# Kernel optimization log

Measured on AMD Instinct MI355X. Metric: run time of the kernel, lower is better.

Reference implementation:

```python
import jax, jax.numpy as jnp
import numpy as np

HID = 32      # STGAT hidden_dim
HEADS = 8
NHID = HID // HEADS  # per-head hidden = 4
NEG_SLOPE = 0.2


def lstm_layer(x, Wih, Whh, bih, bhh):
    # x: (BN, T, H_in); torch gate order i, f, g, o
    BN = x.shape[0]
    H = Whh.shape[1]
    b = bih + bhh

    def step(carry, xt):
        h, c = carry
        z = xt @ Wih.T + h @ Whh.T + b
        i, f, g, o = jnp.split(z, 4, axis=-1)
        c = jax.nn.sigmoid(f) * c + jax.nn.sigmoid(i) * jnp.tanh(g)
        h = jax.nn.sigmoid(o) * jnp.tanh(c)
        return (h, c), h

    h0 = jnp.zeros((BN, H), x.dtype)
    _, ys = jax.lax.scan(step, (h0, h0), jnp.swapaxes(x, 0, 1))
    return jnp.swapaxes(ys, 0, 1)  # (BN, T, H)


def setup_inputs():
    key = jax.random.key(0)
    ks = jax.random.split(key, 16)
    B, N, T_in, F_in = 8, 300, 12, 3
    T_out, F_out = 12, 3
    X = jax.random.normal(ks[0], (B, N, T_in, F_in), jnp.float32)
    adj = (jax.random.uniform(ks[1], (N, N)) < 0.05).astype(jnp.float32)
    A_hat = jnp.maximum(adj, jnp.eye(N, dtype=jnp.float32))  # self-loops

    def init(k, shape, fan):
        return jax.random.normal(k, shape, jnp.float32) / np.float32(np.sqrt(fan))

    W_gat = init(ks[2], (HID, F_in), F_in)          # linear (no bias)
    a_attn = init(ks[3], (2 * NHID,), 2 * NHID)     # attn (no bias), flattened (1, 2*nhid)
    W_ih0 = init(ks[4], (4 * HID, HID), HID)
    W_hh0 = init(ks[5], (4 * HID, HID), HID)
    b_ih0 = init(ks[6], (4 * HID,), HID)
    b_hh0 = init(ks[7], (4 * HID,), HID)
    W_ih1 = init(ks[8], (4 * HID, HID), HID)
    W_hh1 = init(ks[9], (4 * HID, HID), HID)
    b_ih1 = init(ks[10], (4 * HID,), HID)
    b_hh1 = init(ks[11], (4 * HID,), HID)
    fc_W = init(ks[12], (F_out * T_out, HID), HID)
    fc_b = init(ks[13], (F_out * T_out,), HID)
    return {"A_hat": A_hat, "X": X, "W_gat": W_gat, "a_attn": a_attn,
            "W_ih0": W_ih0, "W_hh0": W_hh0, "b_ih0": b_ih0, "b_hh0": b_hh0,
            "W_ih1": W_ih1, "W_hh1": W_hh1, "b_ih1": b_ih1, "b_hh1": b_hh1,
            "fc_W": fc_W, "fc_b": fc_b}


def reference(A_hat, X, W_gat, a_attn, W_ih0, W_hh0, b_ih0, b_hh0,
              W_ih1, W_hh1, b_ih1, b_hh1, fc_W, fc_b):
    B, N, T, F = X.shape
    T_out = fc_W.shape[0] // F  # nums_feature_output == F here

    # --- GAT, vectorized over (batch, timestep) ---
    # g: (B, N, T, HEADS, NHID)
    g = (X @ W_gat.T).reshape(B, N, T, HEADS, NHID)
    a_l, a_r = a_attn[:NHID], a_attn[NHID:]
    # attn(g_concat) = a_l . g_i + a_r . g_j  (exact split of the concat+linear)
    gl = jnp.einsum('bithd,d->bith', g, a_l)
    gr = jnp.einsum('bjthd,d->bjth', g, a_r)
    e = jax.nn.leaky_relu(gl[:, :, None] + gr[:, None, :], NEG_SLOPE)  # (B,i,j,T,H)
    mask = (A_hat == 0)[None, :, :, None, None]
    e = jnp.where(mask, -jnp.inf, e)
    a = jax.nn.softmax(e, axis=2)  # softmax over j (dim=1 of the (i,j,h) tensor)
    h_gat = jnp.einsum('bijth,bjthd->bithd', a, g).reshape(B, N, T, HID)

    # --- 2-layer LSTM over time, per (b, n) sequence ---
    lstm_in = h_gat.reshape(B * N, T, HID)
    h1 = lstm_layer(lstm_in, W_ih0, W_hh0, b_ih0, b_hh0)
    h2 = lstm_layer(h1, W_ih1, W_hh1, b_ih1, b_hh1)
    h_last = h2[:, -1, :]  # (B*N, HID)

    out = h_last @ fc_W.T + fc_b
    return out.reshape(B, N, T_out, F)
```

## Files before the change

kernel.cpp:

```cpp
#include <hip/hip_runtime.h>

typedef __attribute__((ext_vector_type(8))) short s8v;
typedef __attribute__((ext_vector_type(4))) float f4v;

__device__ __forceinline__ float sgm(float x) { return 1.f / (1.f + __expf(-x)); }
__device__ __forceinline__ float tanhq(float x) { return 2.f / (1.f + __expf(-2.f*x)) - 1.f; }
__device__ __forceinline__ void bsplit(float x, short& hi, short& lo) {
    unsigned u = __float_as_uint(x);
    unsigned hb = u & 0xffff0000u;
    hi = (short)(hb >> 16);
    float r = x - __uint_as_float(hb);
    lo = (short)(__float_as_uint(r) >> 16);
}
__device__ __forceinline__ float dppadd1(float x) {
    return x + __uint_as_float(__builtin_amdgcn_mov_dpp(__float_as_uint(x), 0xB1, 0xF, 0xF, true));
}
__device__ __forceinline__ float dppadd2(float x) {
    return x + __uint_as_float(__builtin_amdgcn_mov_dpp(__float_as_uint(x), 0x4E, 0xF, 0xF, true));
}

#define SQ 5

__device__ __forceinline__ void zA2(const short* vh, const short* vl,
    const s8v (&ah)[2][2], const s8v (&al)[2][2], const f4v (&bias)[2],
    int boff, int g, f4v& dA, f4v& dB)
{
    s8v bh0 = *(const s8v*)((const char*)vh + boff +      g*16);
    s8v bh1 = *(const s8v*)((const char*)vh + boff + 64 + g*16);
    s8v bl0 = *(const s8v*)((const char*)vl + boff +      g*16);
    s8v bl1 = *(const s8v*)((const char*)vl + boff + 64 + g*16);
    dA = bias[0];
    dA = __builtin_amdgcn_mfma_f32_16x16x32_bf16(ah[0][0], bh0, dA, 0, 0, 0);
    dA = __builtin_amdgcn_mfma_f32_16x16x32_bf16(ah[0][1], bh1, dA, 0, 0, 0);
    dA = __builtin_amdgcn_mfma_f32_16x16x32_bf16(al[0][0], bh0, dA, 0, 0, 0);
    dA = __builtin_amdgcn_mfma_f32_16x16x32_bf16(al[0][1], bh1, dA, 0, 0, 0);
    dA = __builtin_amdgcn_mfma_f32_16x16x32_bf16(ah[0][0], bl0, dA, 0, 0, 0);
    dA = __builtin_amdgcn_mfma_f32_16x16x32_bf16(ah[0][1], bl1, dA, 0, 0, 0);
    dB = bias[1];
    dB = __builtin_amdgcn_mfma_f32_16x16x32_bf16(ah[1][0], bh0, dB, 0, 0, 0);
    dB = __builtin_amdgcn_mfma_f32_16x16x32_bf16(ah[1][1], bh1, dB, 0, 0, 0);
    dB = __builtin_amdgcn_mfma_f32_16x16x32_bf16(al[1][0], bh0, dB, 0, 0, 0);
    dB = __builtin_amdgcn_mfma_f32_16x16x32_bf16(al[1][1], bh1, dB, 0, 0, 0);
    dB = __builtin_amdgcn_mfma_f32_16x16x32_bf16(ah[1][0], bl0, dB, 0, 0, 0);
    dB = __builtin_amdgcn_mfma_f32_16x16x32_bf16(ah[1][1], bl1, dB, 0, 0, 0);
}

__global__ __launch_bounds__(512, 4) void k_stgat(
    const float* __restrict__ A,    const float* __restrict__ X,
    const float* __restrict__ Wg,   const float* __restrict__ aat,
    const float* __restrict__ Wih0, const float* __restrict__ Whh0,
    const float* __restrict__ bih0, const float* __restrict__ bhh0,
    const float* __restrict__ Wih1, const float* __restrict__ Whh1,
    const float* __restrict__ bih1, const float* __restrict__ bhh1,
    const float* __restrict__ fcW,  const float* __restrict__ fcb,
    float* __restrict__ out)
{
    __shared__ int   snbr[SQ][64];
    __shared__ int   scnt[SQ];
    __shared__ float shg[SQ*384];
    __shared__ __align__(16) char uarea[43200];

    const int tid  = threadIdx.x;
    const int w    = tid >> 6;
    const int l    = tid & 63;
    const int seq0 = blockIdx.x * SQ;
    const int b    = seq0 / 300, i0 = seq0 - b*300;

    float* Xs = (float*)uarea;

    {
        const float* Xg = X + (size_t)b * 10800;
        for (int x = tid; x < 10800; x += 512) Xs[x] = Xg[x];
    }
    if (w < SQ) {
        int i = i0 + w;
        int c = 0;
        for (int j0 = 0; j0 < 300; j0 += 64) {
            int j = j0 + l;
            bool p = (j < 300) && (A[i*300 + j] != 0.f);
            unsigned long long m = __ballot(p);
            if (p) {
                int pos = __popcll(m & ((1ull << l) - 1ull));
                if (c + pos < 64) snbr[w][c + pos] = j;
            }
            c += __popcll(m);
        }
        if (c > 64) c = 64;
        if (l == 0) scnt[w] = c;
    }
    __syncthreads();

    {
        const int hh = l >> 3, j8 = l & 7, dd = j8 & 3;
        float wal0=0.f, wal1=0.f, wal2=0.f, war0=0.f, war1=0.f, war2=0.f;
        #pragma unroll
        for (int d4 = 0; d4 < 4; d4++) {
            float av = aat[d4], bv = aat[4+d4];
            const float* wr = Wg + (hh*4+d4)*3;
            wal0 += wr[0]*av; wal1 += wr[1]*av; wal2 += wr[2]*av;
            war0 += wr[0]*bv; war1 += wr[1]*bv; war2 += wr[2]*bv;
        }
        const float* wp = Wg + (hh*4+dd)*3;
        float wp0 = wp[0], wp1 = wp[1], wp2 = wp[2];

        for (int u = 7 - w; u < SQ*12; u += 8) {
            int us = u / 12, t = u - us*12;
            int i = i0 + us;
            int c = scnt[us];

            const float* Xi = Xs + i*36 + t*3;
            float gl = Xi[0]*wal0 + Xi[1]*wal1 + Xi[2]*wal2;

            float s = 0.f, a0 = 0.f, a1 = 0.f, a2 = 0.f;
            for (int kk = j8; kk < c; kk += 8) {
                int j = snbr[us][kk];
                const float* Xj = Xs + j*36 + t*3;
                float y0 = Xj[0], y1 = Xj[1], y2 = Xj[2];
                float e = gl + y0*war0 + y1*war1 + y2*war2;
                e = e > 0.f ? e : 0.2f*e;
                float wt = __expf(e);
                s += wt; a0 += wt*y0; a1 += wt*y1; a2 += wt*y2;
            }
            s  = dppadd1(s);  a0 = dppadd1(a0); a1 = dppadd1(a1); a2 = dppadd1(a2);
            s  = dppadd2(s);  a0 = dppadd2(a0); a1 = dppadd2(a1); a2 = dppadd2(a2);
            s  += __shfl_xor(s, 4, 64);
            a0 += __shfl_xor(a0, 4, 64);
            a1 += __shfl_xor(a1, 4, 64);
            a2 += __shfl_xor(a2, 4, 64);
            if (j8 < 4)
                shg[us*384 + t*32 + hh*4 + dd] = (a0*wp0 + a1*wp1 + a2*wp2) / s;
        }
    }

    const int n16 = l & 15;
    const int g   = l >> 4;
    const int cA  = w*8 + g;
    const int cB  = w*8 + 4 + g;
    s8v a0h[2][2], a0l[2][2], a1h[2][2], a1l[2][2];
    f4v bias0[2], bias1[2];
    if (w < 4) {
        #pragma unroll
        for (int tau = 0; tau < 2; tau++) {
            const int arow = (n16 & 3)*32 + w*8 + tau*4 + (n16 >> 2);
            const float* s00 = Wih0 + arow*32 + g*8;
            const float* s01 = Whh0 + arow*32 + g*8;
            const float* s10 = Wih1 + arow*32 + g*8;
            const float* s11 = Whh1 + arow*32 + g*8;
            #pragma unroll
            for (int j = 0; j < 8; j++) {
                short hh2, ll2;
                bsplit(s00[j], hh2, ll2); a0h[tau][0][j]=hh2; a0l[tau][0][j]=ll2;
                bsplit(s01[j], hh2, ll2); a0h[tau][1][j]=hh2; a0l[tau][1][j]=ll2;
                bsplit(s10[j], hh2, ll2); a1h[tau][0][j]=hh2; a1l[tau][0][j]=ll2;
                bsplit(s11[j], hh2, ll2); a1h[tau][1][j]=hh2; a1l[tau][1][j]=ll2;
            }
            const int cell = w*8 + tau*4 + g;
            #pragma unroll
            for (int r = 0; r < 4; r++) {
                bias0[tau][r] = bih0[r*32+cell] + bhh0[r*32+cell];
                bias1[tau][r] = bih1[r*32+cell] + bhh1[r*32+cell];
            }
        }
    }
    __syncthreads();

    short* vh0 = (short*)uarea;
    short* vl0 = vh0 + 16*72;
    short* vh1 = vl0 + 16*72;
    short* vl1 = vh1 + 16*72;
    float* sh1f = (float*)(vl1 + 16*72);

    {
        unsigned* vz = (unsigned*)uarea;
        for (int x = tid; x < 2304; x += 512) vz[x] = 0;
    }
    __syncthreads();
    if (tid >= 256 && tid < 416) {
        int us = (tid - 256) >> 5, uc = tid & 31;
        short hh2, ll2; bsplit(shg[us*384 + uc], hh2, ll2);
        vh0[us*72 + uc] = hh2;  vl0[us*72 + uc] = ll2;
    }
    __syncthreads();

    const int boff = n16 * 144;
    float c0A = 0.f, c0B = 0.f, c1A = 0.f, c1B = 0.f;

    auto cellup = [&](f4v z, float& cs) -> float {
        cs = sgm(z[1])*cs + sgm(z[0])*tanhq(z[2]);
        return sgm(z[3])*tanhq(cs);
    };
    auto wr_h0 = [&](float hv, int c) {
        short hh2, ll2; bsplit(hv, hh2, ll2);
        vh0[n16*72 + 32 + c] = hh2;  vl0[n16*72 + 32 + c] = ll2;
        vh1[n16*72 + c]      = hh2;  vl1[n16*72 + c]      = ll2;
    };
    auto wr_h1 = [&](float hv, int c) {
        short hh2, ll2; bsplit(hv, hh2, ll2);
        vh1[n16*72 + 32 + c] = hh2;  vl1[n16*72 + 32 + c] = ll2;
    };

    {
        f4v zpA, zpB;
        if (w < 4) zA2(vh0, vl0, a0h, a0l, bias0, boff, g, zpA, zpB);
        __syncthreads();
        if (w < 4) {
            wr_h0(cellup(zpA, c0A), cA);
            wr_h0(cellup(zpB, c0B), cB);
        }
        if (tid >= 256 && tid < 416) {
            int us = (tid - 256) >> 5, uc = tid & 31;
            short hh2, ll2; bsplit(shg[us*384 + 32 + uc], hh2, ll2);
            vh0[us*72 + uc] = hh2;  vl0[us*72 + uc] = ll2;
        }
        __syncthreads();
    }

    for (int t = 0; t < 12; t++) {
        f4v z1A, z1B, z0A, z0B;
        if (w < 4) {
            zA2(vh1, vl1, a1h, a1l, bias1, boff, g, z1A, z1B);
            if (t < 11)
                zA2(vh0, vl0, a0h, a0l, bias0, boff, g, z0A, z0B);
        }
        __syncthreads();
        if (w < 4) {
            float h1a = cellup(z1A, c1A);
            float h1b = cellup(z1B, c1B);
            wr_h1(h1a, cA);  wr_h1(h1b, cB);
            if (t == 11) {
                if (n16 < SQ) { sh1f[n16*32 + cA] = h1a; sh1f[n16*32 + cB] = h1b; }
            } else {
                wr_h0(cellup(z0A, c0A), cA);
                wr_h0(cellup(z0B, c0B), cB);
            }
        }
        if (tid >= 256 && tid < 416 && t < 10) {
            int us = (tid - 256) >> 5, uc = tid & 31;
            short hh2, ll2; bsplit(shg[us*384 + (t+2)*32 + uc], hh2, ll2);
            vh0[us*72 + uc] = hh2;  vl0[us*72 + uc] = ll2;
        }
        __syncthreads();
    }

    if (tid < SQ*36) {
        int s = tid / 36, r = tid - s*36;
        float acc = fcb[r];
        #pragma unroll
        for (int c4 = 0; c4 < 8; c4++) {
            float4 uv = *(const float4*)&fcW[r*32 + 4*c4];
            acc += uv.x*sh1f[s*32+4*c4+0] + uv.y*sh1f[s*32+4*c4+1]
                 + uv.z*sh1f[s*32+4*c4+2] + uv.w*sh1f[s*32+4*c4+3];
        }
        out[(seq0 + s)*36 + r] = acc;
    }
}

extern "C" void kernel_launch(void* const* d_in, const int* in_sizes, int n_in,
                              void* d_out, int out_size, void* d_ws, size_t ws_size,
                              hipStream_t stream)
{
    const float* A    = (const float*)d_in[0];
    const float* X    = (const float*)d_in[1];
    const float* Wg   = (const float*)d_in[2];
    const float* aat  = (const float*)d_in[3];
    const float* Wih0 = (const float*)d_in[4];
    const float* Whh0 = (const float*)d_in[5];
    const float* bih0 = (const float*)d_in[6];
    const float* bhh0 = (const float*)d_in[7];
    const float* Wih1 = (const float*)d_in[8];
    const float* Whh1 = (const float*)d_in[9];
    const float* bih1 = (const float*)d_in[10];
    const float* bhh1 = (const float*)d_in[11];
    const float* fcW  = (const float*)d_in[12];
    const float* fcb  = (const float*)d_in[13];
    float* out = (float*)d_out;

    k_stgat<<<480, 512, 0, stream>>>(A, X, Wg, aat,
                                     Wih0, Whh0, bih0, bhh0,
                                     Wih1, Whh1, bih1, bhh1,
                                     fcW, fcb, out);
}
```

Measured before the change: 36.82 us.

## Split LSTM layers across warp groups with double-buffered hidden-state staging

Instead of waves 0-3 computing both LSTM layers while waves 4-7 sit idle, waves 0-3 now run layer 0 and waves 4-7 run layer 1 concurrently, each holding only one layer's split-bf16 weights. The hidden-state LDS buffers are double-buffered by parity, so each wavefront step needs one barrier instead of two. This should halve the per-step MFMA and cell-update work per wave and cut barriers. The cost is doubled LDS for the state buffers and more duplicate stores, since layer-0 output is written into both layers' buffers.

```diff
diff --git a/kernel.cpp b/kernel.cpp
--- a/kernel.cpp
+++ b/kernel.cpp
@@ -132,114 +132,114 @@
         }
     }
 
-    const int n16 = l & 15;
-    const int g   = l >> 4;
-    const int cA  = w*8 + g;
-    const int cB  = w*8 + 4 + g;
-    s8v a0h[2][2], a0l[2][2], a1h[2][2], a1l[2][2];
-    f4v bias0[2], bias1[2];
-    if (w < 4) {
+    const int n16   = l & 15;
+    const int g     = l >> 4;
+    const int wl    = w & 3;
+    const int layer = w >> 2;
+    const int cA    = wl*8 + g;
+    const int cB    = wl*8 + 4 + g;
+    s8v ah[2][2], al[2][2];
+    f4v bias[2];
+    {
+        const float* Wih = layer ? Wih1 : Wih0;
+        const float* Whh = layer ? Whh1 : Whh0;
+        const float* bi  = layer ? bih1 : bih0;
+        const float* bh  = layer ? bhh1 : bhh0;
         #pragma unroll
         for (int tau = 0; tau < 2; tau++) {
-            const int arow = (n16 & 3)*32 + w*8 + tau*4 + (n16 >> 2);
-            const float* s00 = Wih0 + arow*32 + g*8;
-            const float* s01 = Whh0 + arow*32 + g*8;
-            const float* s10 = Wih1 + arow*32 + g*8;
-            const float* s11 = Whh1 + arow*32 + g*8;
+            const int arow = (n16 & 3)*32 + wl*8 + tau*4 + (n16 >> 2);
+            const float* si = Wih + arow*32 + g*8;
+            const float* sh = Whh + arow*32 + g*8;
             #pragma unroll
             for (int j = 0; j < 8; j++) {
-                short hh2, ll2;
-                bsplit(s00[j], hh2, ll2); a0h[tau][0][j]=hh2; a0l[tau][0][j]=ll2;
-                bsplit(s01[j], hh2, ll2); a0h[tau][1][j]=hh2; a0l[tau][1][j]=ll2;
-                bsplit(s10[j], hh2, ll2); a1h[tau][0][j]=hh2; a1l[tau][0][j]=ll2;
-                bsplit(s11[j], hh2, ll2); a1h[tau][1][j]=hh2; a1l[tau][1][j]=ll2;
-            }
-            const int cell = w*8 + tau*4 + g;
+                short h2, l2;
+                bsplit(si[j], h2, l2); ah[tau][0][j]=h2; al[tau][0][j]=l2;
+                bsplit(sh[j], h2, l2); ah[tau][1][j]=h2; al[tau][1][j]=l2;
+            }
+            const int cell = wl*8 + tau*4 + g;
             #pragma unroll
-            for (int r = 0; r < 4; r++) {
-                bias0[tau][r] = bih0[r*32+cell] + bhh0[r*32+cell];
-                bias1[tau][r] = bih1[r*32+cell] + bhh1[r*32+cell];
-            }
-        }
-    }
-    __syncthreads();
-
-    short* vh0 = (short*)uarea;
-    short* vl0 = vh0 + 16*72;
-    short* vh1 = vl0 + 16*72;
-    short* vl1 = vh1 + 16*72;
-    float* sh1f = (float*)(vl1 + 16*72);
-
-    {
-        unsigned* vz = (unsigned*)uarea;
-        for (int x = tid; x < 2304; x += 512) vz[x] = 0;
-    }
-    __syncthreads();
-    if (tid >= 256 && tid < 416) {
-        int us = (tid - 256) >> 5, uc = tid & 31;
-        short hh2, ll2; bsplit(shg[us*384 + uc], hh2, ll2);
-        vh0[us*72 + uc] = hh2;  vl0[us*72 + uc] = ll2;
+            for (int r = 0; r < 4; r++)
+                bias[tau][r] = bi[r*32+cell] + bh[r*32+cell];
+        }
+    }
+    __syncthreads();
+
+    short* vb = (short*)uarea;
+    float* sh1f = (float*)(vb + 8*1152);
+    #define VOFF(buf, lay, hl) ((((buf)*2 + (lay))*2 + (hl))*1152)
+
+    { unsigned* vz = (unsigned*)uarea; for (int x = tid; x < 4608; x += 512) vz[x] = 0; }
+    __syncthreads();
+    if (tid < SQ*32) {
+        int us = tid >> 5, uc = tid & 31;
+        short h2, l2; bsplit(shg[us*384 + uc], h2, l2);
+        vb[VOFF(0,0,0) + us*72 + uc] = h2;  vb[VOFF(0,0,1) + us*72 + uc] = l2;
     }
     __syncthreads();
 
     const int boff = n16 * 144;
-    float c0A = 0.f, c0B = 0.f, c1A = 0.f, c1B = 0.f;
+    float csA = 0.f, csB = 0.f;
+    int cur = 0;
 
     auto cellup = [&](f4v z, float& cs) -> float {
         cs = sgm(z[1])*cs + sgm(z[0])*tanhq(z[2]);
         return sgm(z[3])*tanhq(cs);
     };
-    auto wr_h0 = [&](float hv, int c) {
-        short hh2, ll2; bsplit(hv, hh2, ll2);
-        vh0[n16*72 + 32 + c] = hh2;  vl0[n16*72 + 32 + c] = ll2;
-        vh1[n16*72 + c]      = hh2;  vl1[n16*72 + c]      = ll2;
-    };
-    auto wr_h1 = [&](float hv, int c) {
-        short hh2, ll2; bsplit(hv, hh2, ll2);
-        vh1[n16*72 + 32 + c] = hh2;  vl1[n16*72 + 32 + c] = ll2;
-    };
-
-    {
-        f4v zpA, zpB;
-        if (w < 4) zA2(vh0, vl0, a0h, a0l, bias0, boff, g, zpA, zpB);
+
+    {
+        if (layer == 0) {
+            f4v zAa, zBb;
+            zA2(vb + VOFF(0,0,0), vb + VOFF(0,0,1), ah, al, bias, boff, g, zAa, zBb);
+            float hA = cellup(zAa, csA);
+            float hB = cellup(zBb, csB);
+            short h2, l2;
+            bsplit(hA, h2, l2);
+            vb[VOFF(1,0,0) + n16*72 + 32 + cA] = h2;  vb[VOFF(1,0,1) + n16*72 + 32 + cA] = l2;
+            vb[VOFF(1,1,0) + n16*72 + cA]      = h2;  vb[VOFF(1,1,1) + n16*72 + cA]      = l2;
+            bsplit(hB, h2, l2);
+            vb[VOFF(1,0,0) + n16*72 + 32 + cB] = h2;  vb[VOFF(1,0,1) + n16*72 + 32 + cB] = l2;
+            vb[VOFF(1,1,0) + n16*72 + cB]      = h2;  vb[VOFF(1,1,1) + n16*72 + cB]      = l2;
+        }
+        if (tid < SQ*32) {
+            int us = tid >> 5, uc = tid & 31;
+            short h2, l2; bsplit(shg[us*384 + 32 + uc], h2, l2);
+            vb[VOFF(1,0,0) + us*72 + uc] = h2;  vb[VOFF(1,0,1) + us*72 + uc] = l2;
+        }
         __syncthreads();
-        if (w < 4) {
-            wr_h0(cellup(zpA, c0A), cA);
-            wr_h0(cellup(zpB, c0B), cB);
-        }
-        if (tid >= 256 && tid < 416) {
-            int us = (tid - 256) >> 5, uc = tid & 31;
-            short hh2, ll2; bsplit(shg[us*384 + 32 + uc], hh2, ll2);
-            vh0[us*72 + uc] = hh2;  vl0[us*72 + uc] = ll2;
+        cur = 1;
+    }
+
+    for (int p = 0; p < 12; p++) {
+        const int nxt = cur ^ 1;
+        const bool active = (layer == 1) || (p < 11);
+        if (active) {
+            f4v zAa, zBb;
+            zA2(vb + VOFF(cur,layer,0), vb + VOFF(cur,layer,1), ah, al, bias, boff, g, zAa, zBb);
+            float hA = cellup(zAa, csA);
+            float hB = cellup(zBb, csB);
+            short h2, l2;
+            if (layer == 0) {
+                bsplit(hA, h2, l2);
+                vb[VOFF(nxt,0,0) + n16*72 + 32 + cA] = h2;  vb[VOFF(nxt,0,1) + n16*72 + 32 + cA] = l2;
+                vb[VOFF(nxt,1,0) + n16*72 + cA]      = h2;  vb[VOFF(nxt,1,1) + n16*72 + cA]      = l2;
+                bsplit(hB, h2, l2);
+                vb[VOFF(nxt,0,0) + n16*72 + 32 + cB] = h2;  vb[VOFF(nxt,0,1) + n16*72 + 32 + cB] = l2;
+                vb[VOFF(nxt,1,0) + n16*72 + cB]      = h2;  vb[VOFF(nxt,1,1) + n16*72 + cB]      = l2;
+            } else {
+                bsplit(hA, h2, l2);
+                vb[VOFF(nxt,1,0) + n16*72 + 32 + cA] = h2;  vb[VOFF(nxt,1,1) + n16*72 + 32 + cA] = l2;
+                bsplit(hB, h2, l2);
+                vb[VOFF(nxt,1,0) + n16*72 + 32 + cB] = h2;  vb[VOFF(nxt,1,1) + n16*72 + 32 + cB] = l2;
+                if (p == 11 && n16 < SQ) { sh1f[n16*32 + cA] = hA; sh1f[n16*32 + cB] = hB; }
+            }
+        }
+        if (tid < SQ*32 && p + 2 < 12) {
+            int us = tid >> 5, uc = tid & 31;
+            short h2, l2; bsplit(shg[us*384 + (p+2)*32 + uc], h2, l2);
+            vb[VOFF(nxt,0,0) + us*72 + uc] = h2;  vb[VOFF(nxt,0,1) + us*72 + uc] = l2;
         }
         __syncthreads();
-    }
-
-    for (int t = 0; t < 12; t++) {
-        f4v z1A, z1B, z0A, z0B;
-        if (w < 4) {
-            zA2(vh1, vl1, a1h, a1l, bias1, boff, g, z1A, z1B);
-            if (t < 11)
-                zA2(vh0, vl0, a0h, a0l, bias0, boff, g, z0A, z0B);
-        }
-        __syncthreads();
-        if (w < 4) {
-            float h1a = cellup(z1A, c1A);
-            float h1b = cellup(z1B, c1B);
-            wr_h1(h1a, cA);  wr_h1(h1b, cB);
-            if (t == 11) {
-                if (n16 < SQ) { sh1f[n16*32 + cA] = h1a; sh1f[n16*32 + cB] = h1b; }
-            } else {
-                wr_h0(cellup(z0A, c0A), cA);
-                wr_h0(cellup(z0B, c0B), cB);
-            }
-        }
-        if (tid >= 256 && tid < 416 && t < 10) {
-            int us = (tid - 256) >> 5, uc = tid & 31;
-            short hh2, ll2; bsplit(shg[us*384 + (t+2)*32 + uc], hh2, ll2);
-            vh0[us*72 + uc] = hh2;  vl0[us*72 + uc] = ll2;
-        }
-        __syncthreads();
+        cur = nxt;
     }
 
     if (tid < SQ*36) {
```

Measured after the change: 36.37 us (median of 2 runs). No clear change (-1.2%).

## Process 16 sequences per block with per-layer LSTM wavefronts and fewer blocks

Applied to the files above, without the earlier changes.

Each block now handles 16 node sequences instead of 5, launching 152 blocks instead of 480. LSTM layer 0 and layer 1 each run on a single wavefront that holds all gate weights in registers, pipelined through a double-buffered hidden-state exchange in shared memory. The X staging copy into LDS is dropped in favour of direct global reads in the GAT stage. The design fills the MFMA N=16 columns with real sequences to cut redundant weight loading and bsplit work, but it serializes the recurrence onto two wavefronts, uses fewer blocks than there are CUs, and raises register pressure.

```diff
diff --git a/kernel.cpp b/kernel.cpp
--- a/kernel.cpp
+++ b/kernel.cpp
@@ -19,33 +19,9 @@
     return x + __uint_as_float(__builtin_amdgcn_mov_dpp(__float_as_uint(x), 0x4E, 0xF, 0xF, true));
 }
 
-#define SQ 5
-
-__device__ __forceinline__ void zA2(const short* vh, const short* vl,
-    const s8v (&ah)[2][2], const s8v (&al)[2][2], const f4v (&bias)[2],
-    int boff, int g, f4v& dA, f4v& dB)
-{
-    s8v bh0 = *(const s8v*)((const char*)vh + boff +      g*16);
-    s8v bh1 = *(const s8v*)((const char*)vh + boff + 64 + g*16);
-    s8v bl0 = *(const s8v*)((const char*)vl + boff +      g*16);
-    s8v bl1 = *(const s8v*)((const char*)vl + boff + 64 + g*16);
-    dA = bias[0];
-    dA = __builtin_amdgcn_mfma_f32_16x16x32_bf16(ah[0][0], bh0, dA, 0, 0, 0);
-    dA = __builtin_amdgcn_mfma_f32_16x16x32_bf16(ah[0][1], bh1, dA, 0, 0, 0);
-    dA = __builtin_amdgcn_mfma_f32_16x16x32_bf16(al[0][0], bh0, dA, 0, 0, 0);
-    dA = __builtin_amdgcn_mfma_f32_16x16x32_bf16(al[0][1], bh1, dA, 0, 0, 0);
-    dA = __builtin_amdgcn_mfma_f32_16x16x32_bf16(ah[0][0], bl0, dA, 0, 0, 0);
-    dA = __builtin_amdgcn_mfma_f32_16x16x32_bf16(ah[0][1], bl1, dA, 0, 0, 0);
-    dB = bias[1];
-    dB = __builtin_amdgcn_mfma_f32_16x16x32_bf16(ah[1][0], bh0, dB, 0, 0, 0);
-    dB = __builtin_amdgcn_mfma_f32_16x16x32_bf16(ah[1][1], bh1, dB, 0, 0, 0);
-    dB = __builtin_amdgcn_mfma_f32_16x16x32_bf16(al[1][0], bh0, dB, 0, 0, 0);
-    dB = __builtin_amdgcn_mfma_f32_16x16x32_bf16(al[1][1], bh1, dB, 0, 0, 0);
-    dB = __builtin_amdgcn_mfma_f32_16x16x32_bf16(ah[1][0], bl0, dB, 0, 0, 0);
-    dB = __builtin_amdgcn_mfma_f32_16x16x32_bf16(ah[1][1], bl1, dB, 0, 0, 0);
-}
-
-__global__ __launch_bounds__(512, 4) void k_stgat(
+#define NSQ 16
+
+__global__ __launch_bounds__(512, 1) void k_stgat(
     const float* __restrict__ A,    const float* __restrict__ X,
     const float* __restrict__ Wg,   const float* __restrict__ aat,
     const float* __restrict__ Wih0, const float* __restrict__ Whh0,
@@ -55,38 +31,68 @@
     const float* __restrict__ fcW,  const float* __restrict__ fcb,
     float* __restrict__ out)
 {
-    __shared__ int   snbr[SQ][64];
-    __shared__ int   scnt[SQ];
-    __shared__ float shg[SQ*384];
-    __shared__ __align__(16) char uarea[43200];
-
-    const int tid  = threadIdx.x;
-    const int w    = tid >> 6;
-    const int l    = tid & 63;
-    const int seq0 = blockIdx.x * SQ;
-    const int b    = seq0 / 300, i0 = seq0 - b*300;
-
-    float* Xs = (float*)uarea;
-
-    {
-        const float* Xg = X + (size_t)b * 10800;
-        for (int x = tid; x < 10800; x += 512) Xs[x] = Xg[x];
-    }
-    if (w < SQ) {
-        int i = i0 + w;
-        int c = 0;
-        for (int j0 = 0; j0 < 300; j0 += 64) {
-            int j = j0 + l;
-            bool p = (j < 300) && (A[i*300 + j] != 0.f);
-            unsigned long long m = __ballot(p);
-            if (p) {
-                int pos = __popcll(m & ((1ull << l) - 1ull));
-                if (c + pos < 64) snbr[w][c + pos] = j;
-            }
-            c += __popcll(m);
-        }
-        if (c > 64) c = 64;
-        if (l == 0) scnt[w] = c;
+    __shared__ int      snbr[NSQ][64];
+    __shared__ int      scnt[NSQ];
+    __shared__ float    shg[NSQ*389];
+    __shared__ float    sbias[2][4][8][4];
+    __shared__ unsigned hbuf[2][64][8];
+    __shared__ float    sh1f[NSQ*33];
+
+    const int tid = threadIdx.x;
+    const int w   = tid >> 6;
+    const int l   = tid & 63;
+    const int bq  = blockIdx.x;
+    const int b   = bq / 19;
+    const int blk = bq - b*19;
+    const int i0  = blk * 16;
+    const int ns  = (i0 + 16 <= 300) ? 16 : (300 - i0);
+    const float* Xb = X + (size_t)b * 10800;
+
+    const int n16 = l & 15;
+    const int g   = l >> 4;
+
+    s8v aih_h[8], aih_l[8], ahh_h[8], ahh_l[8];
+    if (w < 2) {
+        const float* Wih = w ? Wih1 : Wih0;
+        const float* Whh = w ? Whh1 : Whh0;
+        const float* bi  = w ? bih1 : bih0;
+        const float* bh_ = w ? bhh1 : bhh0;
+        #pragma unroll
+        for (int tau = 0; tau < 8; tau++) {
+            const int arow = (n16 & 3)*32 + ((n16 >> 2) << 3) + tau;
+            const float* si = Wih + arow*32 + g*8;
+            const float* sh = Whh + arow*32 + g*8;
+            #pragma unroll
+            for (int j = 0; j < 8; j++) {
+                short h2, l2;
+                bsplit(si[j], h2, l2); aih_h[tau][j] = h2; aih_l[tau][j] = l2;
+                bsplit(sh[j], h2, l2); ahh_h[tau][j] = h2; ahh_l[tau][j] = l2;
+            }
+        }
+        #pragma unroll
+        for (int q = 0; q < 2; q++) {
+            int idx = l*2 + q;
+            int gg = idx >> 5, tt = (idx & 31) >> 2, rr = idx & 3;
+            int rowb = rr*32 + gg*8 + tt;
+            sbias[w][gg][tt][rr] = bi[rowb] + bh_[rowb];
+        }
+    } else {
+        for (int r = w - 2; r < ns; r += 6) {
+            int i = i0 + r;
+            int c = 0;
+            for (int j0 = 0; j0 < 300; j0 += 64) {
+                int j = j0 + l;
+                bool p = (j < 300) && (A[i*300 + j] != 0.f);
+                unsigned long long m = __ballot(p);
+                if (p) {
+                    int pos = __popcll(m & ((1ull << l) - 1ull));
+                    if (c + pos < 64) snbr[r][c + pos] = j;
+                }
+                c += __popcll(m);
+            }
+            if (c > 64) c = 64;
+            if (l == 0) scnt[r] = c;
+        }
     }
     __syncthreads();
 
@@ -103,18 +109,19 @@
         const float* wp = Wg + (hh*4+dd)*3;
         float wp0 = wp[0], wp1 = wp[1], wp2 = wp[2];
 
-        for (int u = 7 - w; u < SQ*12; u += 8) {
+        const int nu = ns * 12;
+        for (int u = w; u < nu; u += 8) {
             int us = u / 12, t = u - us*12;
             int i = i0 + us;
             int c = scnt[us];
-
-            const float* Xi = Xs + i*36 + t*3;
+            const float* Xi = Xb + i*36 + t*3;
             float gl = Xi[0]*wal0 + Xi[1]*wal1 + Xi[2]*wal2;
 
             float s = 0.f, a0 = 0.f, a1 = 0.f, a2 = 0.f;
+            #pragma unroll 2
             for (int kk = j8; kk < c; kk += 8) {
                 int j = snbr[us][kk];
-                const float* Xj = Xs + j*36 + t*3;
+                const float* Xj = Xb + j*36 + t*3;
                 float y0 = Xj[0], y1 = Xj[1], y2 = Xj[2];
                 float e = gl + y0*war0 + y1*war1 + y2*war2;
                 e = e > 0.f ? e : 0.2f*e;
@@ -128,130 +135,107 @@
             a1 += __shfl_xor(a1, 4, 64);
             a2 += __shfl_xor(a2, 4, 64);
             if (j8 < 4)
-                shg[us*384 + t*32 + hh*4 + dd] = (a0*wp0 + a1*wp1 + a2*wp2) / s;
-        }
-    }
-
-    const int n16 = l & 15;
-    const int g   = l >> 4;
-    const int cA  = w*8 + g;
-    const int cB  = w*8 + 4 + g;
-    s8v a0h[2][2], a0l[2][2], a1h[2][2], a1l[2][2];
-    f4v bias0[2], bias1[2];
-    if (w < 4) {
-        #pragma unroll
-        for (int tau = 0; tau < 2; tau++) {
-            const int arow = (n16 & 3)*32 + w*8 + tau*4 + (n16 >> 2);
-            const float* s00 = Wih0 + arow*32 + g*8;
-            const float* s01 = Whh0 + arow*32 + g*8;
-            const float* s10 = Wih1 + arow*32 + g*8;
-            const float* s11 = Whh1 + arow*32 + g*8;
+                shg[us*389 + t*32 + hh*4 + dd] = (a0*wp0 + a1*wp1 + a2*wp2) / s;
+        }
+    }
+    __syncthreads();
+
+    float cst[8];
+    #pragma unroll
+    for (int t8 = 0; t8 < 8; t8++) cst[t8] = 0.f;
+    s8v hp_h, hp_l;
+    #pragma unroll
+    for (int j = 0; j < 8; j++) { hp_h[j] = 0; hp_l[j] = 0; }
+    float h1fin[8];
+
+    auto zstep = [&](int L, s8v v0h, s8v v0l, s8v v1h, s8v v1l, float* hnew) {
+        #pragma unroll
+        for (int tau = 0; tau < 8; tau++) {
+            f4v acc = *(const f4v*)&sbias[L][g][tau][0];
+            acc = __builtin_amdgcn_mfma_f32_16x16x32_bf16(aih_h[tau], v0h, acc, 0, 0, 0);
+            acc = __builtin_amdgcn_mfma_f32_16x16x32_bf16(ahh_h[tau], v1h, acc, 0, 0, 0);
+            acc = __builtin_amdgcn_mfma_f32_16x16x32_bf16(aih_l[tau], v0h, acc, 0, 0, 0);
+            acc = __builtin_amdgcn_mfma_f32_16x16x32_bf16(ahh_l[tau], v1h, acc, 0, 0, 0);
+            acc = __builtin_amdgcn_mfma_f32_16x16x32_bf16(aih_h[tau], v0l, acc, 0, 0, 0);
+            acc = __builtin_amdgcn_mfma_f32_16x16x32_bf16(ahh_h[tau], v1l, acc, 0, 0, 0);
+            cst[tau] = sgm(acc[1])*cst[tau] + sgm(acc[0])*tanhq(acc[2]);
+            hnew[tau] = sgm(acc[3])*tanhq(cst[tau]);
+        }
+    };
+    auto xfrag = [&](int t, s8v& xh, s8v& xl) {
+        const float* xp = &shg[n16*389 + t*32 + g*8];
+        #pragma unroll
+        for (int j = 0; j < 8; j++) {
+            short h2, l2; bsplit(xp[j], h2, l2);
+            xh[j] = h2; xl[j] = l2;
+        }
+    };
+    auto packwrite = [&](const float* hv, int buf) {
+        #pragma unroll
+        for (int j = 0; j < 8; j++) { short h2, l2; bsplit(hv[j], h2, l2); hp_h[j] = h2; hp_l[j] = l2; }
+        #pragma unroll
+        for (int j2 = 0; j2 < 4; j2++) {
+            hbuf[buf][l][j2]   = ((unsigned)(unsigned short)hp_h[2*j2]) |
+                                 (((unsigned)(unsigned short)hp_h[2*j2+1]) << 16);
+            hbuf[buf][l][4+j2] = ((unsigned)(unsigned short)hp_l[2*j2]) |
+                                 (((unsigned)(unsigned short)hp_l[2*j2+1]) << 16);
+        }
+    };
+
+    if (w == 0) {
+        s8v xh, xl; xfrag(0, xh, xl);
+        float hnew[8];
+        zstep(0, xh, xl, hp_h, hp_l, hnew);
+        packwrite(hnew, 0);
+    }
+    __syncthreads();
+
+    for (int p = 0; p < 12; p++) {
+        if (w == 0) {
+            if (p < 11) {
+                s8v xh, xl; xfrag(p+1, xh, xl);
+                float hnew[8];
+                zstep(0, xh, xl, hp_h, hp_l, hnew);
+                packwrite(hnew, (p+1) & 1);
+            }
+        } else if (w == 1) {
+            s8v bh, bl;
             #pragma unroll
-            for (int j = 0; j < 8; j++) {
-                short hh2, ll2;
-                bsplit(s00[j], hh2, ll2); a0h[tau][0][j]=hh2; a0l[tau][0][j]=ll2;
-                bsplit(s01[j], hh2, ll2); a0h[tau][1][j]=hh2; a0l[tau][1][j]=ll2;
-                bsplit(s10[j], hh2, ll2); a1h[tau][0][j]=hh2; a1l[tau][0][j]=ll2;
-                bsplit(s11[j], hh2, ll2); a1h[tau][1][j]=hh2; a1l[tau][1][j]=ll2;
-            }
-            const int cell = w*8 + tau*4 + g;
+            for (int j2 = 0; j2 < 4; j2++) {
+                unsigned qh = hbuf[p & 1][l][j2], ql = hbuf[p & 1][l][4+j2];
+                bh[2*j2] = (short)(qh & 0xFFFF); bh[2*j2+1] = (short)(qh >> 16);
+                bl[2*j2] = (short)(ql & 0xFFFF); bl[2*j2+1] = (short)(ql >> 16);
+            }
+            float hnew[8];
+            zstep(1, bh, bl, hp_h, hp_l, hnew);
             #pragma unroll
-            for (int r = 0; r < 4; r++) {
-                bias0[tau][r] = bih0[r*32+cell] + bhh0[r*32+cell];
-                bias1[tau][r] = bih1[r*32+cell] + bhh1[r*32+cell];
-            }
-        }
-    }
-    __syncthreads();
-
-    short* vh0 = (short*)uarea;
-    short* vl0 = vh0 + 16*72;
-    short* vh1 = vl0 + 16*72;
-    short* vl1 = vh1 + 16*72;
-    float* sh1f = (float*)(vl1 + 16*72);
-
-    {
-        unsigned* vz = (unsigned*)uarea;
-        for (int x = tid; x < 2304; x += 512) vz[x] = 0;
-    }
-    __syncthreads();
-    if (tid >= 256 && tid < 416) {
-        int us = (tid - 256) >> 5, uc = tid & 31;
-        short hh2, ll2; bsplit(shg[us*384 + uc], hh2, ll2);
-        vh0[us*72 + uc] = hh2;  vl0[us*72 + uc] = ll2;
-    }
-    __syncthreads();
-
-    const int boff = n16 * 144;
-    float c0A = 0.f, c0B = 0.f, c1A = 0.f, c1B = 0.f;
-
-    auto cellup = [&](f4v z, float& cs) -> float {
-        cs = sgm(z[1])*cs + sgm(z[0])*tanhq(z[2]);
-        return sgm(z[3])*tanhq(cs);
-    };
-    auto wr_h0 = [&](float hv, int c) {
-        short hh2, ll2; bsplit(hv, hh2, ll2);
-        vh0[n16*72 + 32 + c] = hh2;  vl0[n16*72 + 32 + c] = ll2;
-        vh1[n16*72 + c]      = hh2;  vl1[n16*72 + c]      = ll2;
-    };
-    auto wr_h1 = [&](float hv, int c) {
-        short hh2, ll2; bsplit(hv, hh2, ll2);
-        vh1[n16*72 + 32 + c] = hh2;  vl1[n16*72 + 32 + c] = ll2;
-    };
-
-    {
-        f4v zpA, zpB;
-        if (w < 4) zA2(vh0, vl0, a0h, a0l, bias0, boff, g, zpA, zpB);
+            for (int j = 0; j < 8; j++) { short h2, l2; bsplit(hnew[j], h2, l2); hp_h[j] = h2; hp_l[j] = l2; }
+            if (p == 11) {
+                #pragma unroll
+                for (int j = 0; j < 8; j++) h1fin[j] = hnew[j];
+            }
+        }
         __syncthreads();
-        if (w < 4) {
-            wr_h0(cellup(zpA, c0A), cA);
-            wr_h0(cellup(zpB, c0B), cB);
-        }
-        if (tid >= 256 && tid < 416) {
-            int us = (tid - 256) >> 5, uc = tid & 31;
-            short hh2, ll2; bsplit(shg[us*384 + 32 + uc], hh2, ll2);
-            vh0[us*72 + uc] = hh2;  vl0[us*72 + uc] = ll2;
-        }
-        __syncthreads();
-    }
-
-    for (int t = 0; t < 12; t++) {
-        f4v z1A, z1B, z0A, z0B;
-        if (w < 4) {
-            zA2(vh1, vl1, a1h, a1l, bias1, boff, g, z1A, z1B);
-            if (t < 11)
-                zA2(vh0, vl0, a0h, a0l, bias0, boff, g, z0A, z0B);
-        }
-        __syncthreads();
-        if (w < 4) {
-            float h1a = cellup(z1A, c1A);
-            float h1b = cellup(z1B, c1B);
-            wr_h1(h1a, cA);  wr_h1(h1b, cB);
-            if (t == 11) {
-                if (n16 < SQ) { sh1f[n16*32 + cA] = h1a; sh1f[n16*32 + cB] = h1b; }
-            } else {
-                wr_h0(cellup(z0A, c0A), cA);
-                wr_h0(cellup(z0B, c0B), cB);
-            }
-        }
-        if (tid >= 256 && tid < 416 && t < 10) {
-            int us = (tid - 256) >> 5, uc = tid & 31;
-            short hh2, ll2; bsplit(shg[us*384 + (t+2)*32 + uc], hh2, ll2);
-            vh0[us*72 + uc] = hh2;  vl0[us*72 + uc] = ll2;
-        }
-        __syncthreads();
-    }
-
-    if (tid < SQ*36) {
-        int s = tid / 36, r = tid - s*36;
+    }
+
+    if (w == 1) {
+        #pragma unroll
+        for (int tau = 0; tau < 8; tau++)
+            sh1f[n16*33 + g*8 + tau] = h1fin[tau];
+    }
+    __syncthreads();
+
+    for (int o = tid; o < ns*36; o += 512) {
+        int s = o / 36, r = o - s*36;
         float acc = fcb[r];
+        const float* hrow = &sh1f[s*33];
         #pragma unroll
         for (int c4 = 0; c4 < 8; c4++) {
             float4 uv = *(const float4*)&fcW[r*32 + 4*c4];
-            acc += uv.x*sh1f[s*32+4*c4+0] + uv.y*sh1f[s*32+4*c4+1]
-                 + uv.z*sh1f[s*32+4*c4+2] + uv.w*sh1f[s*32+4*c4+3];
-        }
-        out[(seq0 + s)*36 + r] = acc;
+            acc += uv.x*hrow[4*c4+0] + uv.y*hrow[4*c4+1]
+                 + uv.z*hrow[4*c4+2] + uv.w*hrow[4*c4+3];
+        }
+        out[(b*300 + i0 + s)*36 + r] = acc;
     }
 }
 
@@ -275,7 +259,7 @@
     const float* fcb  = (const float*)d_in[13];
     float* out = (float*)d_out;
 
-    k_stgat<<<480, 512, 0, stream>>>(A, X, Wg, aat,
+    k_stgat<<<152, 512, 0, stream>>>(A, X, Wg, aat,
                                      Wih0, Whh0, bih0, bhh0,
                                      Wih1, Whh1, bih1, bhh1,
                                      fcW, fcb, out);
```

Result: slower. 52.13 us (+41.6%).
